# Performance work log

Measured on AMD Instinct MI355X. Metric: run time of the kernel, lower is better.

## Reference

```python
import jax, jax.numpy as jnp
import numpy as np

B, D, R, T = 128, 256, 128, 128  # batch, hidden_dim, num_regions, seq_length


def setup_inputs() -> dict:
    key = jax.random.key(0)
    ks = jax.random.split(key, 16)
    s = 0.02
    inp = {
        "h": jax.random.normal(ks[0], (B, D), dtype=jnp.float32),
        # Linear weights stored as [in, out] (y = x @ W + b), transpose of torch layout
        "Wq": jax.random.normal(ks[1], (D, D), dtype=jnp.float32) * s,
        "bq": jnp.zeros((D,), jnp.float32),
        "Wk": jax.random.normal(ks[2], (D, D), dtype=jnp.float32) * s,
        "bk": jnp.zeros((D,), jnp.float32),
        "Wc": jax.random.normal(ks[3], (D * D, D), dtype=jnp.float32) * s,  # context_proj
        "bc": jnp.zeros((D,), jnp.float32),
        "Wa": jax.random.normal(ks[4], (D, R), dtype=jnp.float32) * s,      # action_proj
        "ba": jnp.zeros((R,), jnp.float32),
        # GRUCell params, torch layout: weight_ih [3D, D] (r|z|n), weight_hh [3D, D]
        "W_ih": jax.random.normal(ks[5], (3 * D, D), dtype=jnp.float32) * s,
        "W_hh": jax.random.normal(ks[6], (3 * D, D), dtype=jnp.float32) * s,
        "b_ih": jnp.zeros((3 * D,), jnp.float32),
        "b_hh": jnp.zeros((3 * D,), jnp.float32),
    }
    return inp


def _forward(h, Wq, bq, Wk, bk, Wc, bc, Wa, ba, W_ih, W_hh, b_ih, b_hh):
    query = h @ Wq + bq                      # [B, D]
    key_v = h @ Wk + bk                      # [B, D]

    # context = bmm(query[:, :, None], key[:, None, :]) is identical every step
    # (query/key are loop-invariant), so compute context_embed once and broadcast.
    context = query[:, :, None] * key_v[:, None, :]          # [B, D, D]
    context_embed = context.reshape(B, D * D) @ Wc + bc      # [B, D]
    s_list = jnp.broadcast_to(context_embed[:, None, :], (B, T, D))

    # GRU input is the loop-invariant key -> precompute input gates once.
    x_gates = key_v @ W_ih.T + b_ih                          # [B, 3D]
    xr, xz, xn = jnp.split(x_gates, 3, axis=-1)

    region_ids = jnp.arange(R)

    def step(carry, _):
        hidden, used = carry                                  # [B,D], [B,R] bool
        logits = hidden @ Wa + ba                             # [B, R]
        masked = jnp.where(used, -jnp.inf, logits)
        # argmax(softmax(masked)) == argmax(masked)
        action = jnp.argmax(masked, axis=-1)                  # [B]
        used_new = used | (region_ids[None, :] == action[:, None])
        # GRUCell(key, hidden)
        h_gates = hidden @ W_hh.T + b_hh
        hr, hz, hn = jnp.split(h_gates, 3, axis=-1)
        r = jax.nn.sigmoid(xr + hr)
        z = jax.nn.sigmoid(xz + hz)
        n = jnp.tanh(xn + r * hn)
        hidden_new = (1.0 - z) * n + z * hidden
        return (hidden_new, used_new), (action, masked, hidden)

    used0 = jnp.zeros((B, R), dtype=bool)
    _, (actions, mask_scores, h_traj) = jax.lax.scan(step, (h, used0), None, length=T)

    actions = actions.T                                       # [B, T]
    mask_scores = jnp.transpose(mask_scores, (1, 0, 2))       # [B, T, R]
    h_list = jnp.transpose(h_traj, (1, 0, 2))                 # [B, T, D]
    c_list = h_list                                           # c_list appends same tensor
    return actions, mask_scores, s_list, h_list, c_list


def reference(h, Wq, bq, Wk, bk, Wc, bc, Wa, ba, W_ih, W_hh, b_ih, b_hh):
    return _forward(h, Wq, bq, Wk, bk, Wc, bc, Wa, ba, W_ih, W_hh, b_ih, b_hh)
```

## Files before the change

kernel.cpp:

```cpp
#include <hip/hip_runtime.h>
#include <math.h>

#define BB 128
#define DD 256
#define RR 128
#define TT 128
#define G3 768

#define DREG 64
#define DLDS 48
#define DSTR 144

#define MASKED_SENTINEL -3.0e38f

__global__ __launch_bounds__(256) void k_prep(
    const float* __restrict__ h,
    const float* __restrict__ Wq, const float* __restrict__ bq,
    const float* __restrict__ Wk, const float* __restrict__ bk,
    float* __restrict__ q, float* __restrict__ k)
{
    __shared__ float hl[DD];
    const int b = blockIdx.x, t = threadIdx.x;
    hl[t] = h[b * DD + t];
    __syncthreads();
    float aq = bq[t], ak = bk[t];
#pragma unroll 8
    for (int d = 0; d < DD; ++d) {
        const float hd = hl[d];
        aq = fmaf(hd, Wq[d * DD + t], aq);
        ak = fmaf(hd, Wk[d * DD + t], ak);
    }
    q[b * DD + t] = aq;
    k[b * DD + t] = ak;
}

__global__ __launch_bounds__(1024) void k_transpose(
    const float* __restrict__ W_hh, const float* __restrict__ W_ih,
    float4* __restrict__ Wt4, float* __restrict__ Wih_t)
{
    const int e = blockIdx.x * 1024 + threadIdx.x;
    if (e < 64 * G3) {
        const int i4 = e / G3, g = e % G3;
        Wt4[e] = *(const float4*)&W_hh[(size_t)g * DD + 4 * i4];
    } else {
        const int e2 = e - 64 * G3;
        const int d = e2 / G3, g = e2 % G3;
        Wih_t[e2] = W_ih[(size_t)g * DD + d];
    }
}

__global__ __launch_bounds__(512) void k_ctx1(
    const float* __restrict__ q, const float* __restrict__ k,
    const float* __restrict__ Wc, float* __restrict__ partial)
{
    __shared__ float kl[2][32][257];
    const int i = blockIdx.x;
    const int o = threadIdx.x & 255, ph = threadIdx.x >> 8;
    const float* __restrict__ Wci = Wc + (size_t)i * DD * DD;
    for (int p = 0; p < 2; ++p) {
        const int b0 = ph * 64 + p * 32;
        __syncthreads();
#pragma unroll
        for (int r2 = 0; r2 < 32; ++r2) kl[ph][r2][o] = k[(b0 + r2) * DD + o];
        __syncthreads();
        float acc[32];
#pragma unroll
        for (int bb = 0; bb < 32; ++bb) acc[bb] = 0.f;
#pragma unroll 4
        for (int j = 0; j < DD; ++j) {
            const float w = Wci[j * DD + o];
#pragma unroll
            for (int bb = 0; bb < 32; ++bb)
                acc[bb] = fmaf(kl[ph][bb][j], w, acc[bb]);
        }
#pragma unroll
        for (int bb = 0; bb < 32; ++bb)
            partial[((size_t)i * BB + (b0 + bb)) * DD + o] =
                acc[bb] * q[(b0 + bb) * DD + i];
    }
}

__global__ __launch_bounds__(256) void k_ctx2(
    const float* __restrict__ partial, const float* __restrict__ bc,
    float* __restrict__ s_out)
{
    const int b = blockIdx.x, o = threadIdx.x;
    float s = bc[o];
#pragma unroll 8
    for (int i = 0; i < DD; ++i)
        s += partial[((size_t)i * BB + b) * DD + o];
    float* __restrict__ dst = s_out + (size_t)b * TT * DD + o;
#pragma unroll 4
    for (int t = 0; t < TT; ++t) dst[(size_t)t * DD] = s;
}

__global__ __launch_bounds__(768) void k_gru(
    const float* __restrict__ h0, const float* __restrict__ kv_g,
    const float* __restrict__ b_ih, const float* __restrict__ b_hh,
    const float4* __restrict__ Wt4, const float* __restrict__ Wih_t,
    float* __restrict__ out_h, float* __restrict__ out_c)
{
    __shared__ __align__(16) float hid[DD];
    __shared__ float xg[G3];
    __shared__ float hg[G3];
    __shared__ float lw[DLDS * G3];

    const int b = blockIdx.x, t = threadIdx.x;

    if (t < DD) hid[t] = h0[b * DD + t];

    float4 wr[16];
#pragma unroll
    for (int c = 0; c < 16; ++c) wr[c] = Wt4[c * G3 + t];

    for (int c = 0; c < 12; ++c) {
        const float4 w = Wt4[(16 + c) * G3 + t];
        lw[(4 * c + 0) * G3 + t] = w.x;
        lw[(4 * c + 1) * G3 + t] = w.y;
        lw[(4 * c + 2) * G3 + t] = w.z;
        lw[(4 * c + 3) * G3 + t] = w.w;
    }

    {
        const float* __restrict__ kvp = kv_g + b * DD;
        float s0 = 0.f, s1 = 0.f, s2 = 0.f, s3 = 0.f;
#pragma unroll 2
        for (int d = 0; d < DD; d += 4) {
            s0 = fmaf(kvp[d + 0], Wih_t[(size_t)(d + 0) * G3 + t], s0);
            s1 = fmaf(kvp[d + 1], Wih_t[(size_t)(d + 1) * G3 + t], s1);
            s2 = fmaf(kvp[d + 2], Wih_t[(size_t)(d + 2) * G3 + t], s2);
            s3 = fmaf(kvp[d + 3], Wih_t[(size_t)(d + 3) * G3 + t], s3);
        }
        xg[t] = b_ih[t] + ((s0 + s1) + (s2 + s3));
    }
    const float bias = b_hh[t];
    const float4* __restrict__ wstr = Wt4 + (size_t)28 * G3 + t;
    __syncthreads();

    for (int step = 0; step < TT; ++step) {
        float a0 = 0.f, a1 = 0.f, a2 = 0.f, a3 = 0.f;
#pragma unroll
        for (int c = 0; c < 16; ++c) {
            const float4 hv = *(const float4*)&hid[4 * c];
            a0 = fmaf(hv.x, wr[c].x, a0);
            a1 = fmaf(hv.y, wr[c].y, a1);
            a2 = fmaf(hv.z, wr[c].z, a2);
            a3 = fmaf(hv.w, wr[c].w, a3);
        }
#pragma unroll 8
        for (int dd = 0; dd < DLDS; ++dd) {
            const float w = lw[dd * G3 + t];
            const float hv = hid[DREG + dd];
            if ((dd & 3) == 0)      a0 = fmaf(hv, w, a0);
            else if ((dd & 3) == 1) a1 = fmaf(hv, w, a1);
            else if ((dd & 3) == 2) a2 = fmaf(hv, w, a2);
            else                    a3 = fmaf(hv, w, a3);
        }
#pragma unroll 6
        for (int c = 0; c < 36; ++c) {
            const float4 w = wstr[(size_t)c * G3];
            const float4 hv = *(const float4*)&hid[DREG + DLDS + 4 * c];
            a0 = fmaf(hv.x, w.x, a0);
            a1 = fmaf(hv.y, w.y, a1);
            a2 = fmaf(hv.z, w.z, a2);
            a3 = fmaf(hv.w, w.w, a3);
        }
        hg[t] = ((a0 + a1) + (a2 + a3)) + bias;
        __syncthreads();

        if (t < DD) {
            const int d = t;
            const float old = hid[d];
            out_h[((size_t)b * TT + step) * DD + d] = old;
            out_c[((size_t)b * TT + step) * DD + d] = old;
            const float rr = 1.f / (1.f + expf(-(xg[d] + hg[d])));
            const float zz = 1.f / (1.f + expf(-(xg[DD + d] + hg[DD + d])));
            const float nn = tanhf(xg[2 * DD + d] + rr * hg[2 * DD + d]);
            hid[d] = (1.f - zz) * nn + zz * old;
        }
        __syncthreads();
    }
}

__global__ __launch_bounds__(256) void k_logits(
    const float* __restrict__ h_list, const float* __restrict__ Wa,
    const float* __restrict__ ba, float* __restrict__ out_mask)
{
    __shared__ float hl[16][DD];
    const int bt0 = blockIdx.x * 16;
    const int t = threadIdx.x, r = t & 127, g = t >> 7;

#pragma unroll
    for (int j = 0; j < 16; ++j)
        hl[j][t] = h_list[(size_t)(bt0 + j) * DD + t];
    __syncthreads();

    float acc[8];
#pragma unroll
    for (int j = 0; j < 8; ++j) acc[j] = 0.f;
#pragma unroll 4
    for (int d = 0; d < DD; ++d) {
        const float w = Wa[(size_t)d * RR + r];
#pragma unroll
        for (int j = 0; j < 8; ++j)
            acc[j] = fmaf(hl[g * 8 + j][d], w, acc[j]);
    }
    const float bar = ba[r];
#pragma unroll
    for (int j = 0; j < 8; ++j)
        out_mask[(size_t)(bt0 + g * 8 + j) * RR + r] = acc[j] + bar;
}

__global__ __launch_bounds__(64) void k_scan(
    float* __restrict__ mask, float* __restrict__ out_act)
{
    const int b = blockIdx.x, lane = threadIdx.x;
    float* __restrict__ mb = mask + (size_t)b * TT * RR;
    bool u0 = false, u1 = false;
    for (int t2 = 0; t2 < TT; ++t2) {
        const float l0 = mb[t2 * RR + lane];
        const float l1 = mb[t2 * RR + 64 + lane];
        mb[t2 * RR + lane]      = u0 ? MASKED_SENTINEL : l0;
        mb[t2 * RR + 64 + lane] = u1 ? MASKED_SENTINEL : l1;
        float v1 = u0 ? -INFINITY : l0;  int i1 = lane;
        const float m1 = u1 ? -INFINITY : l1;
        if (m1 > v1) { v1 = m1; i1 = lane + 64; }
#pragma unroll
        for (int off = 32; off > 0; off >>= 1) {
            const float ov = __shfl_down(v1, off);
            const int   oi = __shfl_down(i1, off);
            if (ov > v1 || (ov == v1 && oi < i1)) { v1 = ov; i1 = oi; }
        }
        const int win = __shfl(i1, 0);
        if (lane == 0) out_act[(size_t)b * TT + t2] = (float)win;
        u0 = u0 || (win == lane);
        u1 = u1 || (win == lane + 64);
    }
}

extern "C" void kernel_launch(void* const* d_in, const int* in_sizes, int n_in,
                              void* d_out, int out_size, void* d_ws, size_t ws_size,
                              hipStream_t stream) {
    const float* h    = (const float*)d_in[0];
    const float* Wq   = (const float*)d_in[1];
    const float* bq   = (const float*)d_in[2];
    const float* Wk   = (const float*)d_in[3];
    const float* bk   = (const float*)d_in[4];
    const float* Wc   = (const float*)d_in[5];
    const float* bc   = (const float*)d_in[6];
    const float* Wa   = (const float*)d_in[7];
    const float* ba   = (const float*)d_in[8];
    const float* W_ih = (const float*)d_in[9];
    const float* W_hh = (const float*)d_in[10];
    const float* b_ih = (const float*)d_in[11];
    const float* b_hh = (const float*)d_in[12];

    float* out = (float*)d_out;
    float* out_act  = out;
    float* out_mask = out + 16384;
    float* out_s    = out + 16384 + 2097152;
    float* out_h    = out + 16384 + 2097152 + 4194304;
    float* out_c    = out_h + 4194304;

    float*  q     = (float*)d_ws;
    float*  k     = q + BB * DD;
    float4* Wt4   = (float4*)(k + BB * DD);
    float*  Wih_t = (float*)(Wt4 + 64 * G3);
    float* partial = out_h;

    k_transpose<<<240, 1024, 0, stream>>>(W_hh, W_ih, Wt4, Wih_t);
    k_prep<<<BB, 256, 0, stream>>>(h, Wq, bq, Wk, bk, q, k);
    k_ctx1<<<DD, 512, 0, stream>>>(q, k, Wc, partial);
    k_ctx2<<<BB, 256, 0, stream>>>(partial, bc, out_s);
    k_gru<<<BB, 768, 0, stream>>>(h, k, b_ih, b_hh, Wt4, Wih_t, out_h, out_c);
    k_logits<<<1024, 256, 0, stream>>>(out_h, Wa, ba, out_mask);
    k_scan<<<BB, 64, 0, stream>>>(out_mask, out_act);
}
```

Before: 1.004 ms.

## Split context kernel across more blocks, stage scan in LDS, spread GRU stores

```diff
diff --git a/kernel.cpp b/kernel.cpp
--- a/kernel.cpp
+++ b/kernel.cpp
@@ -53,31 +53,29 @@
     const float* __restrict__ q, const float* __restrict__ k,
     const float* __restrict__ Wc, float* __restrict__ partial)
 {
-    __shared__ float kl[2][32][257];
-    const int i = blockIdx.x;
+    __shared__ float kl[32][257];
+    const int i = blockIdx.x >> 2, b0 = (blockIdx.x & 3) * 32;
     const int o = threadIdx.x & 255, ph = threadIdx.x >> 8;
     const float* __restrict__ Wci = Wc + (size_t)i * DD * DD;
-    for (int p = 0; p < 2; ++p) {
-        const int b0 = ph * 64 + p * 32;
-        __syncthreads();
-#pragma unroll
-        for (int r2 = 0; r2 < 32; ++r2) kl[ph][r2][o] = k[(b0 + r2) * DD + o];
-        __syncthreads();
-        float acc[32];
-#pragma unroll
-        for (int bb = 0; bb < 32; ++bb) acc[bb] = 0.f;
+
+    for (int r = ph; r < 32; r += 2) kl[r][o] = k[(b0 + r) * DD + o];
+    __syncthreads();
+
+    const int bb0 = ph * 16;
+    float acc[16];
+#pragma unroll
+    for (int bb = 0; bb < 16; ++bb) acc[bb] = 0.f;
 #pragma unroll 4
-        for (int j = 0; j < DD; ++j) {
-            const float w = Wci[j * DD + o];
-#pragma unroll
-            for (int bb = 0; bb < 32; ++bb)
-                acc[bb] = fmaf(kl[ph][bb][j], w, acc[bb]);
-        }
-#pragma unroll
-        for (int bb = 0; bb < 32; ++bb)
-            partial[((size_t)i * BB + (b0 + bb)) * DD + o] =
-                acc[bb] * q[(b0 + bb) * DD + i];
-    }
+    for (int j = 0; j < DD; ++j) {
+        const float w = Wci[j * DD + o];
+#pragma unroll
+        for (int bb = 0; bb < 16; ++bb)
+            acc[bb] = fmaf(kl[bb0 + bb][j], w, acc[bb]);
+    }
+#pragma unroll
+    for (int bb = 0; bb < 16; ++bb)
+        partial[((size_t)i * BB + (b0 + bb0 + bb)) * DD + o] =
+            acc[bb] * q[(b0 + bb0 + bb) * DD + i];
 }
 
 __global__ __launch_bounds__(256) void k_ctx2(
@@ -138,6 +136,9 @@
     __syncthreads();
 
     for (int step = 0; step < TT; ++step) {
+        if (t < 256)      out_h[((size_t)b * TT + step) * DD + t] = hid[t];
+        else if (t < 512) out_c[((size_t)b * TT + step) * DD + (t - 256)] = hid[t - 256];
+
         float a0 = 0.f, a1 = 0.f, a2 = 0.f, a3 = 0.f;
 #pragma unroll
         for (int c = 0; c < 16; ++c) {
@@ -171,8 +172,6 @@
         if (t < DD) {
             const int d = t;
             const float old = hid[d];
-            out_h[((size_t)b * TT + step) * DD + d] = old;
-            out_c[((size_t)b * TT + step) * DD + d] = old;
             const float rr = 1.f / (1.f + expf(-(xg[d] + hg[d])));
             const float zz = 1.f / (1.f + expf(-(xg[DD + d] + hg[DD + d])));
             const float nn = tanhf(xg[2 * DD + d] + rr * hg[2 * DD + d]);
@@ -211,31 +210,43 @@
         out_mask[(size_t)(bt0 + g * 8 + j) * RR + r] = acc[j] + bar;
 }
 
-__global__ __launch_bounds__(64) void k_scan(
+__global__ __launch_bounds__(128) void k_scan(
     float* __restrict__ mask, float* __restrict__ out_act)
 {
-    const int b = blockIdx.x, lane = threadIdx.x;
-    float* __restrict__ mb = mask + (size_t)b * TT * RR;
-    bool u0 = false, u1 = false;
-    for (int t2 = 0; t2 < TT; ++t2) {
-        const float l0 = mb[t2 * RR + lane];
-        const float l1 = mb[t2 * RR + 64 + lane];
-        mb[t2 * RR + lane]      = u0 ? MASKED_SENTINEL : l0;
-        mb[t2 * RR + 64 + lane] = u1 ? MASKED_SENTINEL : l1;
-        float v1 = u0 ? -INFINITY : l0;  int i1 = lane;
-        const float m1 = u1 ? -INFINITY : l1;
-        if (m1 > v1) { v1 = m1; i1 = lane + 64; }
-#pragma unroll
-        for (int off = 32; off > 0; off >>= 1) {
-            const float ov = __shfl_down(v1, off);
-            const int   oi = __shfl_down(i1, off);
-            if (ov > v1 || (ov == v1 && oi < i1)) { v1 = ov; i1 = oi; }
-        }
-        const int win = __shfl(i1, 0);
-        if (lane == 0) out_act[(size_t)b * TT + t2] = (float)win;
-        u0 = u0 || (win == lane);
-        u1 = u1 || (win == lane + 64);
-    }
+    __shared__ float lg[TT * RR];
+    const int b = blockIdx.x, t = threadIdx.x;
+    float4* __restrict__ mb4 = (float4*)(mask + (size_t)b * TT * RR);
+
+    for (int c = t; c < TT * RR / 4; c += 128)
+        ((float4*)lg)[c] = mb4[c];
+    __syncthreads();
+
+    if (t < 64) {
+        bool u0 = false, u1 = false;
+        for (int t2 = 0; t2 < TT; ++t2) {
+            const float l0 = lg[t2 * RR + t];
+            const float l1 = lg[t2 * RR + 64 + t];
+            lg[t2 * RR + t]      = u0 ? MASKED_SENTINEL : l0;
+            lg[t2 * RR + 64 + t] = u1 ? MASKED_SENTINEL : l1;
+            float v1 = u0 ? -INFINITY : l0;  int i1 = t;
+            const float m1 = u1 ? -INFINITY : l1;
+            if (m1 > v1) { v1 = m1; i1 = t + 64; }
+#pragma unroll
+            for (int off = 32; off > 0; off >>= 1) {
+                const float ov = __shfl_down(v1, off);
+                const int   oi = __shfl_down(i1, off);
+                if (ov > v1 || (ov == v1 && oi < i1)) { v1 = ov; i1 = oi; }
+            }
+            const int win = __shfl(i1, 0);
+            if (t == 0) out_act[(size_t)b * TT + t2] = (float)win;
+            u0 = u0 || (win == t);
+            u1 = u1 || (win == t + 64);
+        }
+    }
+    __syncthreads();
+
+    for (int c = t; c < TT * RR / 4; c += 128)
+        mb4[c] = ((float4*)lg)[c];
 }
 
 extern "C" void kernel_launch(void* const* d_in, const int* in_sizes, int n_in,
@@ -270,9 +281,9 @@
 
     k_transpose<<<240, 1024, 0, stream>>>(W_hh, W_ih, Wt4, Wih_t);
     k_prep<<<BB, 256, 0, stream>>>(h, Wq, bq, Wk, bk, q, k);
-    k_ctx1<<<DD, 512, 0, stream>>>(q, k, Wc, partial);
+    k_ctx1<<<1024, 512, 0, stream>>>(q, k, Wc, partial);
     k_ctx2<<<BB, 256, 0, stream>>>(partial, bc, out_s);
     k_gru<<<BB, 768, 0, stream>>>(h, k, b_ih, b_hh, Wt4, Wih_t, out_h, out_c);
     k_logits<<<1024, 256, 0, stream>>>(out_h, Wa, ba, out_mask);
-    k_scan<<<BB, 64, 0, stream>>>(out_mask, out_act);
-}
+    k_scan<<<BB, 128, 0, stream>>>(out_mask, out_act);
+}
```

Result: faster. 894.8 us (-10.9%).
